# Kernel tuning notes

Hardware: AMD Instinct MI355X
Metric: run time of the kernel (lower is better)

## Reference

```python
import jax, jax.numpy as jnp
import numpy as np

H = 4096        # hidden_size
NH = 32         # num_attention_heads
NKV = 8         # num_key_value_heads
HD = H // NH    # head_dim = 128
N_REP = NH // NKV
SCALE = HD ** -0.5


def _rope(x, cos, sin):
    # x: (B, h, S, HD); cos/sin: (S, HD//2) broadcast over batch/heads
    x1 = x[..., 0::2]
    x2 = x[..., 1::2]
    return jnp.concatenate([x1 * cos - x2 * sin, x1 * sin + x2 * cos], axis=-1)


def setup_inputs() -> dict:
    key = jax.random.key(0)
    ks = jax.random.split(key, 9)
    B, S = 2, 2048
    return {
        "hidden_states": jax.random.normal(ks[0], (B, S, H), jnp.float32),
        "cos": jax.random.uniform(ks[1], (S, HD // 2), jnp.float32),
        "sin": jax.random.uniform(ks[2], (S, HD // 2), jnp.float32),
        "Wq": jax.random.normal(ks[3], (H, H), jnp.float32) * (H ** -0.5),
        "Wk": jax.random.normal(ks[4], (NKV * HD, H), jnp.float32) * (H ** -0.5),
        "bk": jax.random.normal(ks[5], (NKV * HD,), jnp.float32) * 0.01,
        "Wv": jax.random.normal(ks[6], (NKV * HD, H), jnp.float32) * (H ** -0.5),
        "bv": jax.random.normal(ks[7], (NKV * HD,), jnp.float32) * 0.01,
        "Wo": jax.random.normal(ks[8], (H, H), jnp.float32) * (H ** -0.5),
    }


def reference(hidden_states, cos, sin, Wq, Wk, bk, Wv, bv, Wo):
    B, S, _ = hidden_states.shape
    # projections (torch Linear: x @ W.T + b)
    q = (hidden_states @ Wq.T).reshape(B, S, NH, HD).transpose(0, 2, 1, 3)
    k = (hidden_states @ Wk.T + bk).reshape(B, S, NKV, HD).transpose(0, 2, 1, 3)
    v = (hidden_states @ Wv.T + bv).reshape(B, S, NKV, HD).transpose(0, 2, 1, 3)
    q = _rope(q, cos, sin)
    k = _rope(k, cos, sin)
    # GQA repeat_kv: (B, NKV, S, HD) -> (B, NH, S, HD)
    k = jnp.repeat(k, N_REP, axis=1)
    v = jnp.repeat(v, N_REP, axis=1)
    # full attention (no mask is actually applied in the source forward)
    scores = jnp.einsum('bhqd,bhkd->bhqk', q, k) * SCALE
    attn = jax.nn.softmax(scores, axis=-1)
    out = jnp.einsum('bhqk,bhkd->bhqd', attn, v)
    out = out.transpose(0, 2, 1, 3).reshape(B, S, H)
    return out @ Wo.T
```

## Files before the change

### kernel.cpp

```cpp
#include <hip/hip_runtime.h>

typedef unsigned short u16;
typedef short short8 __attribute__((ext_vector_type(8)));
typedef float floatx4 __attribute__((ext_vector_type(4)));

#define H_ 4096
#define NH_ 32
#define NKV_ 8
#define HD_ 128
#define SEQ_ 2048
#define BATCH_ 2
#define ROWS_ (BATCH_*SEQ_)
#define KVW_ (NKV_*HD_)
#define NQKV_ (H_ + 2*KVW_)
#define VSTRIDE_ NQKV_
#define SCALE_ 0.08838834764831845f
#define TSCALE_ (SCALE_*1.442695040888963f)

__device__ __forceinline__ u16 f2bf(float f) {
  union { float f; unsigned u; } x; x.f = f;
  unsigned r = x.u + 0x7fffu + ((x.u >> 16) & 1u);
  return (u16)(r >> 16);
}
__device__ __forceinline__ float bf2f(u16 h) {
  union { unsigned u; float f; } x; x.u = ((unsigned)h) << 16;
  return x.f;
}
__device__ __forceinline__ unsigned cvt_pk_bf16(float lo, float hi) {
  unsigned r;
  asm("v_cvt_pk_bf16_f32 %0, %1, %2" : "=v"(r) : "v"(lo), "v"(hi));
  return r;
}

__global__ __launch_bounds__(256) void cvt_f32_bf16(const float* __restrict__ src,
                                                    u16* __restrict__ dst, int n4) {
  int i = blockIdx.x * 256 + threadIdx.x;
  if (i >= n4) return;
  float4 v = ((const float4*)src)[i];
  ushort4 o;
  o.x = f2bf(v.x); o.y = f2bf(v.y); o.z = f2bf(v.z); o.w = f2bf(v.w);
  ((ushort4*)dst)[i] = o;
}

__global__ __launch_bounds__(256) void bias_concat(const float* __restrict__ bk,
                                                   const float* __restrict__ bv,
                                                   float* __restrict__ dst) {
  int i = blockIdx.x * 256 + threadIdx.x;
  if (i >= NQKV_) return;
  float v = 0.f;
  if (i >= H_ + KVW_)      v = bv[i - (H_ + KVW_)];
  else if (i >= H_)        v = bk[i - H_];
  dst[i] = v;
}

template<int BF16_OUT, int HAS_BIAS>
__global__ __launch_bounds__(512, 2) void gemm_nt_8p(const u16* __restrict__ A, const u16* __restrict__ B,
                                                     const float* __restrict__ bias, void* __restrict__ Cout,
                                                     int M, int N, int K)
{
  __shared__ __align__(16) u16 lds[65536];
  char* ldsB = (char*)lds;
  const int tid  = threadIdx.x;
  const int lane = tid & 63;
  const int wave = tid >> 6;
  const int ln   = lane & 15;
  const int quad = lane >> 4;
  const int wm   = wave >> 2;
  const int wn   = wave & 3;

  const int NB  = N >> 8;
  const int nwg = gridDim.x;
  const int cpx = nwg >> 3;
  const int l   = (blockIdx.x & 7) * cpx + (blockIdx.x >> 3);
  const int m0  = (l / NB) * 256;
  const int n0  = (l % NB) * 256;

  const u16* srcp[4][2];
  {
    int ob0 = wave*2048 + lane*16;
#pragma unroll
    for (int h = 0; h < 4; ++h) {
#pragma unroll
      for (int j = 0; j < 2; ++j) {
        int ob  = ob0 + j*1024;
        int row = ob >> 6;
        int sl  = ((ob >> 4) & 3) ^ ((row >> 1) & 3);
        int kst = h >> 1;
        if ((h & 1) == 0) srcp[h][j] = A + (size_t)(m0 + row)*K + kst*32 + sl*8;
        else              srcp[h][j] = B + (size_t)(n0 + row)*K + kst*32 + sl*8;
      }
    }
  }

#define STAGE(h_, p_, kt_)                                                          \
  {                                                                                 \
    __builtin_amdgcn_global_load_lds(                                               \
      (const __attribute__((address_space(1))) void*)(srcp[h_][0] + (kt_)*64),      \
      (__attribute__((address_space(3))) void*)(ldsB + (((h_)&1)*65536 + (p_)*32768 \
          + ((h_)>>1)*16384 + wave*2048)), 16, 0, 0);                               \
    __builtin_amdgcn_global_load_lds(                                               \
      (const __attribute__((address_space(1))) void*)(srcp[h_][1] + (kt_)*64),      \
      (__attribute__((address_space(3))) void*)(ldsB + (((h_)&1)*65536 + (p_)*32768 \
          + ((h_)>>1)*16384 + wave*2048 + 1024)), 16, 0, 0);                        \
  }

  const int slq16 = (quad ^ ((ln >> 1) & 3)) * 16;
  const int aoffL = (wm*128 + ln)*64 + slq16;
  const int boffL = (wn*64  + ln)*64 + slq16;

  floatx4 zf = {0.f, 0.f, 0.f, 0.f};
  floatx4 acc[8][4];
#pragma unroll
  for (int i = 0; i < 8; ++i)
#pragma unroll
    for (int j = 0; j < 4; ++j) acc[i][j] = zf;

  STAGE(0, 0, 0) STAGE(1, 0, 0) STAGE(2, 0, 0) STAGE(3, 0, 0)

  const int NT = K >> 6;
  for (int t = 0; t < NT; ++t) {
    const int p  = t & 1;
    const int np = p ^ 1;
    const char* ab = ldsB + p*32768;
    const char* bb = ldsB + 65536 + p*32768;
    short8 af[4], bq[4];

    asm volatile("s_waitcnt vmcnt(4)");
    __builtin_amdgcn_s_barrier();
    __builtin_amdgcn_sched_barrier(0);
    if (t + 1 < NT) STAGE(0, np, t+1)
#pragma unroll
    for (int j = 0; j < 4; ++j) bq[j] = *(const short8*)(bb + boffL + j*1024);
#pragma unroll
    for (int i = 0; i < 4; ++i) af[i] = *(const short8*)(ab + aoffL + i*1024);
    __builtin_amdgcn_s_setprio(1);
#pragma unroll
    for (int i = 0; i < 4; ++i)
#pragma unroll
      for (int j = 0; j < 4; ++j)
        acc[i][j] = __builtin_amdgcn_mfma_f32_16x16x32_bf16(af[i], bq[j], acc[i][j], 0, 0, 0);
    __builtin_amdgcn_s_setprio(0);

    __builtin_amdgcn_s_barrier();
    if (t + 1 < NT) STAGE(1, np, t+1)
#pragma unroll
    for (int i = 0; i < 4; ++i) af[i] = *(const short8*)(ab + aoffL + (4+i)*1024);
    __builtin_amdgcn_s_setprio(1);
#pragma unroll
    for (int i = 0; i < 4; ++i)
#pragma unroll
      for (int j = 0; j < 4; ++j)
        acc[4+i][j] = __builtin_amdgcn_mfma_f32_16x16x32_bf16(af[i], bq[j], acc[4+i][j], 0, 0, 0);
    __builtin_amdgcn_s_setprio(0);

    if (t + 1 < NT) { asm volatile("s_waitcnt vmcnt(4)"); }
    else            { asm volatile("s_waitcnt vmcnt(0)"); }
    __builtin_amdgcn_s_barrier();
    __builtin_amdgcn_sched_barrier(0);
    if (t + 1 < NT) STAGE(2, np, t+1)
#pragma unroll
    for (int j = 0; j < 4; ++j) bq[j] = *(const short8*)(bb + 16384 + boffL + j*1024);
#pragma unroll
    for (int i = 0; i < 4; ++i) af[i] = *(const short8*)(ab + 16384 + aoffL + i*1024);
    __builtin_amdgcn_s_setprio(1);
#pragma unroll
    for (int i = 0; i < 4; ++i)
#pragma unroll
      for (int j = 0; j < 4; ++j)
        acc[i][j] = __builtin_amdgcn_mfma_f32_16x16x32_bf16(af[i], bq[j], acc[i][j], 0, 0, 0);
    __builtin_amdgcn_s_setprio(0);

    __builtin_amdgcn_s_barrier();
    if (t + 1 < NT) STAGE(3, np, t+1)
#pragma unroll
    for (int i = 0; i < 4; ++i) af[i] = *(const short8*)(ab + 16384 + aoffL + (4+i)*1024);
    __builtin_amdgcn_s_setprio(1);
#pragma unroll
    for (int i = 0; i < 4; ++i)
#pragma unroll
      for (int j = 0; j < 4; ++j)
        acc[4+i][j] = __builtin_amdgcn_mfma_f32_16x16x32_bf16(af[i], bq[j], acc[4+i][j], 0, 0, 0);
    __builtin_amdgcn_s_setprio(0);
  }
#undef STAGE

#pragma unroll
  for (int i = 0; i < 8; ++i) {
#pragma unroll
    for (int j = 0; j < 4; ++j) {
      int row = m0 + wm*128 + i*16 + quad*4;
      int col = n0 + wn*64  + j*16 + ln;
      float bv_ = HAS_BIAS ? bias[col] : 0.f;
#pragma unroll
      for (int r = 0; r < 4; ++r) {
        float v = acc[i][j][r] + bv_;
        if (BF16_OUT) ((u16*)Cout)[(size_t)(row+r)*N + col] = f2bf(v);
        else          ((float*)Cout)[(size_t)(row+r)*N + col] = v;
      }
    }
  }
}

__global__ __launch_bounds__(256) void rope_kernel(const u16* __restrict__ X, u16* __restrict__ Y,
                                                   const float* __restrict__ cosb, const float* __restrict__ sinb,
                                                   int nheads, int total, int istride, int ostride)
{
  int idx = blockIdx.x * 256 + threadIdx.x;
  if (idx >= total) return;
  int d = idx & 63;
  int t = idx >> 6;
  int hh = t % nheads;
  int row = t / nheads;
  int s = row & (SEQ_ - 1);
  size_t bi = (size_t)row * istride + hh * HD_;
  size_t bo = (size_t)row * ostride + hh * HD_;
  float x1 = bf2f(X[bi + 2*d]);
  float x2 = bf2f(X[bi + 2*d + 1]);
  float c  = cosb[s*64 + d];
  float sn = sinb[s*64 + d];
  Y[bo + d]      = f2bf(x1*c - x2*sn);
  Y[bo + 64 + d] = f2bf(x1*sn + x2*c);
}

#define KS_TILE (64*128)

__global__ __launch_bounds__(256, 3) void attn_fwd(const u16* __restrict__ Q, const u16* __restrict__ K,
                                                   const u16* __restrict__ V, u16* __restrict__ O)
{
  __shared__ __align__(16) u16 Ks[2*KS_TILE];
  __shared__ __align__(16) u16 Vt[128*72];
  const int tid  = threadIdx.x;
  const int lane = tid & 63;
  const int wave = tid >> 6;
  const int ln   = lane & 15;
  const int quad = lane >> 4;
  const int bh = blockIdx.y;
  const int b  = bh >> 5;
  const int h  = bh & 31;
  const int kvh = h >> 2;
  const int q0 = blockIdx.x * 128;

  short8 qf[2][4];
#pragma unroll
  for (int mt = 0; mt < 2; ++mt) {
    const u16* qbase = Q + (size_t)(b*SEQ_ + q0 + wave*32 + mt*16 + ln) * H_ + h * HD_;
#pragma unroll
    for (int kst = 0; kst < 4; ++kst)
      qf[mt][kst] = *(const short8*)(qbase + kst*32 + quad*8);
  }

  short8 bones;
  {
    short v1 = (ln == 0) ? (short)0x3F80 : (short)0;
#pragma unroll
    for (int j = 0; j < 8; ++j) bones[j] = v1;
  }

  int kou[4];
  const u16* ks0[4];
#pragma unroll
  for (int i = 0; i < 4; ++i) {
    int ou = wave*4096 + i*1024;
    int ob = ou + lane*16;
    int key = ob >> 8;
    int dgp = (ob >> 4) & 15;
    int dgl = dgp ^ (key & 15);
    kou[i] = ou;
    ks0[i] = K + (size_t)(b*SEQ_ + key)*KVW_ + kvh*HD_ + dgl*8;
  }
  const int g  = tid & 15;
  const int dg = tid >> 4;
  const u16* vs0 = V + (size_t)(b*SEQ_ + g)*VSTRIDE_ + kvh*HD_ + dg*8;
  const int k0v = ((g >> 1) & 1)*32 + (g >> 2)*8 + (g & 1)*4;

  floatx4 zf = {0.f, 0.f, 0.f, 0.f};
  floatx4 o[2][8];
  floatx4 ol[2];
#pragma unroll
  for (int mt = 0; mt < 2; ++mt) {
    ol[mt] = zf;
#pragma unroll
    for (int jt = 0; jt < 8; ++jt) o[mt][jt] = zf;
  }
  float mrow[2] = {-1e30f, -1e30f};

  int4 vreg[4];
#pragma unroll
  for (int i = 0; i < 4; ++i)
    __builtin_amdgcn_global_load_lds((const __attribute__((address_space(1))) void*)ks0[i],
        (__attribute__((address_space(3))) void*)((char*)Ks + kou[i]), 16, 0, 0);
#pragma unroll
  for (int j = 0; j < 4; ++j)
    vreg[j] = *(const int4*)(vs0 + (size_t)(j*16)*VSTRIDE_);
  {
    union { int4 v; u16 u[8]; } w[4];
#pragma unroll
    for (int j = 0; j < 4; ++j) w[j].v = vreg[j];
#pragma unroll
    for (int dd = 0; dd < 8; ++dd) {
      ushort4 t4;
      t4.x = w[0].u[dd]; t4.y = w[1].u[dd]; t4.z = w[2].u[dd]; t4.w = w[3].u[dd];
      *(ushort4*)&Vt[(dg*8 + dd)*72 + k0v] = t4;
    }
  }
  __syncthreads();

  const int NT = SEQ_ / 64;
  for (int t = 0; t < NT; ++t) {
    if (t + 1 < NT) {
      size_t roff = (size_t)(t+1) * 64 * KVW_;
      char* kb = (char*)Ks + ((t+1)&1) * (KS_TILE*2);
#pragma unroll
      for (int i = 0; i < 4; ++i)
        __builtin_amdgcn_global_load_lds((const __attribute__((address_space(1))) void*)(ks0[i] + roff),
            (__attribute__((address_space(3))) void*)(kb + kou[i]), 16, 0, 0);
      size_t voff = (size_t)(t+1) * 64 * VSTRIDE_;
#pragma unroll
      for (int j = 0; j < 4; ++j)
        vreg[j] = *(const int4*)(vs0 + voff + (size_t)(j*16)*VSTRIDE_);
    }
    const u16* Kc = Ks + (t&1)*KS_TILE;

    floatx4 s[2][4];
#pragma unroll
    for (int nt = 0; nt < 4; ++nt) { s[0][nt] = zf; s[1][nt] = zf; }
    __builtin_amdgcn_s_setprio(1);
#pragma unroll
    for (int kst = 0; kst < 4; ++kst) {
      int dgp = (kst*4 + quad) ^ ln;
#pragma unroll
      for (int nt = 0; nt < 4; ++nt) {
        short8 kf = *(const short8*)&Kc[(nt*16 + ln)*128 + dgp*8];
        s[0][nt] = __builtin_amdgcn_mfma_f32_16x16x32_bf16(kf, qf[0][kst], s[0][nt], 0, 0, 0);
        s[1][nt] = __builtin_amdgcn_mfma_f32_16x16x32_bf16(kf, qf[1][kst], s[1][nt], 0, 0, 0);
      }
    }
    __builtin_amdgcn_s_setprio(0);

    float rmv[2];
    bool ok = true;
#pragma unroll
    for (int mt = 0; mt < 2; ++mt) {
      float m0_ = fmaxf(fmaxf(s[mt][0][0], s[mt][0][1]), fmaxf(s[mt][0][2], s[mt][0][3]));
      float m1_ = fmaxf(fmaxf(s[mt][1][0], s[mt][1][1]), fmaxf(s[mt][1][2], s[mt][1][3]));
      float m2_ = fmaxf(fmaxf(s[mt][2][0], s[mt][2][1]), fmaxf(s[mt][2][2], s[mt][2][3]));
      float m3_ = fmaxf(fmaxf(s[mt][3][0], s[mt][3][1]), fmaxf(s[mt][3][2], s[mt][3][3]));
      float rm = fmaxf(fmaxf(m0_, m1_), fmaxf(m2_, m3_)) * TSCALE_;
      rm = fmaxf(rm, __shfl_xor(rm, 16));
      rm = fmaxf(rm, __shfl_xor(rm, 32));
      rmv[mt] = rm;
      ok = ok && (rm - mrow[mt] <= 8.0f);
    }
    if (!__all(ok)) {
#pragma unroll
      for (int mt = 0; mt < 2; ++mt) {
        float mn = fmaxf(mrow[mt], rmv[mt]);
        float al = exp2f(mrow[mt] - mn);
        mrow[mt] = mn;
        float av[4];
#pragma unroll
        for (int r = 0; r < 4; ++r) av[r] = __shfl(al, (lane & 48) | (quad*4 + r));
#pragma unroll
        for (int r = 0; r < 4; ++r) {
          float a_ = av[r];
#pragma unroll
          for (int jt = 0; jt < 8; ++jt) o[mt][jt][r] *= a_;
          ol[mt][r] *= a_;
        }
      }
    }
    short8 pa[2][2];
#pragma unroll
    for (int mt = 0; mt < 2; ++mt) {
      float mn = mrow[mt];
      float p[4][4];
#pragma unroll
      for (int nt = 0; nt < 4; ++nt)
#pragma unroll
        for (int r = 0; r < 4; ++r)
          p[r][nt] = exp2f(fmaf(s[mt][nt][r], TSCALE_, -mn));
#pragma unroll
      for (int k2 = 0; k2 < 2; ++k2) {
        union { unsigned u[4]; short8 v; } pk;
        pk.u[0] = cvt_pk_bf16(p[2*k2][0],   p[2*k2][1]);
        pk.u[1] = cvt_pk_bf16(p[2*k2][2],   p[2*k2][3]);
        pk.u[2] = cvt_pk_bf16(p[2*k2+1][0], p[2*k2+1][1]);
        pk.u[3] = cvt_pk_bf16(p[2*k2+1][2], p[2*k2+1][3]);
        pa[mt][k2] = pk.v;
      }
    }

    __builtin_amdgcn_s_setprio(1);
#pragma unroll
    for (int k2 = 0; k2 < 2; ++k2) {
#pragma unroll
      for (int jt = 0; jt < 8; ++jt) {
        short8 vf = *(const short8*)&Vt[(jt*16 + ln)*72 + k2*32 + quad*8];
        o[0][jt] = __builtin_amdgcn_mfma_f32_16x16x32_bf16(pa[0][k2], vf, o[0][jt], 0, 0, 0);
        o[1][jt] = __builtin_amdgcn_mfma_f32_16x16x32_bf16(pa[1][k2], vf, o[1][jt], 0, 0, 0);
      }
      ol[0] = __builtin_amdgcn_mfma_f32_16x16x32_bf16(pa[0][k2], bones, ol[0], 0, 0, 0);
      ol[1] = __builtin_amdgcn_mfma_f32_16x16x32_bf16(pa[1][k2], bones, ol[1], 0, 0, 0);
    }
    __builtin_amdgcn_s_setprio(0);

    __syncthreads();
    if (t + 1 < NT) {
      union { int4 v; u16 u[8]; } w[4];
#pragma unroll
      for (int j = 0; j < 4; ++j) w[j].v = vreg[j];
#pragma unroll
      for (int dd = 0; dd < 8; ++dd) {
        ushort4 t4;
        t4.x = w[0].u[dd]; t4.y = w[1].u[dd]; t4.z = w[2].u[dd]; t4.w = w[3].u[dd];
        *(ushort4*)&Vt[(dg*8 + dd)*72 + k0v] = t4;
      }
    }
    __syncthreads();
  }

#pragma unroll
  for (int mt = 0; mt < 2; ++mt) {
#pragma unroll
    for (int r = 0; r < 4; ++r) {
      float lv = __shfl(ol[mt][r], lane & 48);
      float inv = 1.f / lv;
      size_t row = (size_t)(b*SEQ_ + q0 + wave*32 + mt*16 + quad*4 + r);
      u16* dst = O + row * H_ + h * HD_ + ln;
#pragma unroll
      for (int jt = 0; jt < 8; ++jt)
        dst[jt*16] = f2bf(o[mt][jt][r] * inv);
    }
  }
}

extern "C" void kernel_launch(void* const* d_in, const int* in_sizes, int n_in,
                              void* d_out, int out_size, void* d_ws, size_t ws_size,
                              hipStream_t stream) {
  const float* hs   = (const float*)d_in[0];
  const float* cosb = (const float*)d_in[1];
  const float* sinb = (const float*)d_in[2];
  const float* Wq   = (const float*)d_in[3];
  const float* Wk   = (const float*)d_in[4];
  const float* bk   = (const float*)d_in[5];
  const float* Wv   = (const float*)d_in[6];
  const float* bv   = (const float*)d_in[7];
  const float* Wo   = (const float*)d_in[8];
  float* out = (float*)d_out;

  char* ws = (char*)d_ws;
  u16*   hs_bf   = (u16*)(ws +          0);
  u16*   Wqkv_bf = (u16*)(ws +   33554432);
  u16*   Wo_bf   = (u16*)(ws +   83886080);
  u16*   QKV0    = (u16*)(ws +  117440512);
  u16*   Qr      = (u16*)(ws +  167772160);
  u16*   Kr      = (u16*)(ws +  201326592);
  float* biasqkv = (float*)(ws + 209715200);
  u16*   Oa      = hs_bf;

  {
    int n;
    n = ROWS_*H_;  cvt_f32_bf16<<<(n/4 + 255)/256, 256, 0, stream>>>(hs, hs_bf, n/4);
    n = H_*H_;     cvt_f32_bf16<<<(n/4 + 255)/256, 256, 0, stream>>>(Wq, Wqkv_bf, n/4);
    n = KVW_*H_;   cvt_f32_bf16<<<(n/4 + 255)/256, 256, 0, stream>>>(Wk, Wqkv_bf + (size_t)H_*H_, n/4);
    n = KVW_*H_;   cvt_f32_bf16<<<(n/4 + 255)/256, 256, 0, stream>>>(Wv, Wqkv_bf + (size_t)(H_+KVW_)*H_, n/4);
    n = H_*H_;     cvt_f32_bf16<<<(n/4 + 255)/256, 256, 0, stream>>>(Wo, Wo_bf, n/4);
    bias_concat<<<(NQKV_ + 255)/256, 256, 0, stream>>>(bk, bv, biasqkv);
  }

  gemm_nt_8p<1,1><<<dim3((ROWS_/256)*(NQKV_/256)), dim3(512), 0, stream>>>(hs_bf, Wqkv_bf, biasqkv, QKV0, ROWS_, NQKV_, H_);
  rope_kernel<<<(ROWS_*NH_*64)/256,  256, 0, stream>>>(QKV0,       Qr, cosb, sinb, NH_,  ROWS_*NH_*64,  NQKV_, H_);
  rope_kernel<<<(ROWS_*NKV_*64)/256, 256, 0, stream>>>(QKV0 + H_,  Kr, cosb, sinb, NKV_, ROWS_*NKV_*64, NQKV_, KVW_);
  attn_fwd<<<dim3(SEQ_/128, BATCH_*NH_), dim3(256), 0, stream>>>(Qr, Kr, QKV0 + H_ + KVW_, Oa);
  gemm_nt_8p<0,0><<<dim3((ROWS_/256)*(H_/256)), dim3(512), 0, stream>>>(Oa, Wo_bf, nullptr, out, ROWS_, H_, H_);
}
```

Measured before the change: 917.3 us.

## Double attention block to 8 waves covering 256 queries with swizzled grid mapping

The attention kernel now launches 512 threads (8 waves) per block, so each block handles 256 query rows and amortizes each K/V tile load over twice as many queries, halving per-thread K and V staging work. The grid is flattened to 512 blocks, and block indices are remapped so that consecutive blocks spread across (batch, head, query-tile) in an interleaved order, presumably for better L2 locality or XCD distribution. The launch bound changes from (256,3) to (512,4), which tightens the register budget and risks spills. There are also fewer blocks for load balancing across CUs.

```diff
diff --git a/kernel.cpp b/kernel.cpp
--- a/kernel.cpp
+++ b/kernel.cpp
@@ -224,7 +224,7 @@
 
 #define KS_TILE (64*128)
 
-__global__ __launch_bounds__(256, 3) void attn_fwd(const u16* __restrict__ Q, const u16* __restrict__ K,
+__global__ __launch_bounds__(512, 4) void attn_fwd(const u16* __restrict__ Q, const u16* __restrict__ K,
                                                    const u16* __restrict__ V, u16* __restrict__ O)
 {
   __shared__ __align__(16) u16 Ks[2*KS_TILE];
@@ -234,11 +234,12 @@
   const int wave = tid >> 6;
   const int ln   = lane & 15;
   const int quad = lane >> 4;
-  const int bh = blockIdx.y;
-  const int b  = bh >> 5;
-  const int h  = bh & 31;
+  const int lin = (blockIdx.x & 7) * 64 + (blockIdx.x >> 3);
+  const int bh  = lin >> 3;
+  const int b   = bh >> 5;
+  const int h   = bh & 31;
   const int kvh = h >> 2;
-  const int q0 = blockIdx.x * 128;
+  const int q0  = (lin & 7) * 256;
 
   short8 qf[2][4];
 #pragma unroll
@@ -256,11 +257,11 @@
     for (int j = 0; j < 8; ++j) bones[j] = v1;
   }
 
-  int kou[4];
-  const u16* ks0[4];
-#pragma unroll
-  for (int i = 0; i < 4; ++i) {
-    int ou = wave*4096 + i*1024;
+  int kou[2];
+  const u16* ks0[2];
+#pragma unroll
+  for (int i = 0; i < 2; ++i) {
+    int ou = wave*2048 + i*1024;
     int ob = ou + lane*16;
     int key = ob >> 8;
     int dgp = (ob >> 4) & 15;
@@ -269,9 +270,10 @@
     ks0[i] = K + (size_t)(b*SEQ_ + key)*KVW_ + kvh*HD_ + dgl*8;
   }
   const int g  = tid & 15;
-  const int dg = tid >> 4;
-  const u16* vs0 = V + (size_t)(b*SEQ_ + g)*VSTRIDE_ + kvh*HD_ + dg*8;
-  const int k0v = ((g >> 1) & 1)*32 + (g >> 2)*8 + (g & 1)*4;
+  const int dg = (tid >> 4) & 15;
+  const int j2 = tid >> 8;
+  const u16* vs0 = V + (size_t)(b*SEQ_ + j2*32 + g)*VSTRIDE_ + kvh*HD_ + dg*8;
+  const int k0v = ((g >> 1) & 1)*32 + (g >> 2)*8 + (g & 1)*4 + j2*2;
 
   floatx4 zf = {0.f, 0.f, 0.f, 0.f};
   floatx4 o[2][8];
@@ -284,23 +286,21 @@
   }
   float mrow[2] = {-1e30f, -1e30f};
 
-  int4 vreg[4];
-#pragma unroll
-  for (int i = 0; i < 4; ++i)
+  int4 vreg[2];
+#pragma unroll
+  for (int i = 0; i < 2; ++i)
     __builtin_amdgcn_global_load_lds((const __attribute__((address_space(1))) void*)ks0[i],
         (__attribute__((address_space(3))) void*)((char*)Ks + kou[i]), 16, 0, 0);
 #pragma unroll
-  for (int j = 0; j < 4; ++j)
-    vreg[j] = *(const int4*)(vs0 + (size_t)(j*16)*VSTRIDE_);
+  for (int jj = 0; jj < 2; ++jj)
+    vreg[jj] = *(const int4*)(vs0 + (size_t)(jj*16)*VSTRIDE_);
   {
-    union { int4 v; u16 u[8]; } w[4];
-#pragma unroll
-    for (int j = 0; j < 4; ++j) w[j].v = vreg[j];
+    union { int4 v; u16 u[8]; } w[2];
+    w[0].v = vreg[0]; w[1].v = vreg[1];
 #pragma unroll
     for (int dd = 0; dd < 8; ++dd) {
-      ushort4 t4;
-      t4.x = w[0].u[dd]; t4.y = w[1].u[dd]; t4.z = w[2].u[dd]; t4.w = w[3].u[dd];
-      *(ushort4*)&Vt[(dg*8 + dd)*72 + k0v] = t4;
+      ushort2 t2; t2.x = w[0].u[dd]; t2.y = w[1].u[dd];
+      *(ushort2*)&Vt[(dg*8 + dd)*72 + k0v] = t2;
     }
   }
   __syncthreads();
@@ -311,13 +311,13 @@
       size_t roff = (size_t)(t+1) * 64 * KVW_;
       char* kb = (char*)Ks + ((t+1)&1) * (KS_TILE*2);
 #pragma unroll
-      for (int i = 0; i < 4; ++i)
+      for (int i = 0; i < 2; ++i)
         __builtin_amdgcn_global_load_lds((const __attribute__((address_space(1))) void*)(ks0[i] + roff),
             (__attribute__((address_space(3))) void*)(kb + kou[i]), 16, 0, 0);
       size_t voff = (size_t)(t+1) * 64 * VSTRIDE_;
 #pragma unroll
-      for (int j = 0; j < 4; ++j)
-        vreg[j] = *(const int4*)(vs0 + voff + (size_t)(j*16)*VSTRIDE_);
+      for (int jj = 0; jj < 2; ++jj)
+        vreg[jj] = *(const int4*)(vs0 + voff + (size_t)(jj*16)*VSTRIDE_);
     }
     const u16* Kc = Ks + (t&1)*KS_TILE;
 
@@ -406,14 +406,12 @@
 
     __syncthreads();
     if (t + 1 < NT) {
-      union { int4 v; u16 u[8]; } w[4];
-#pragma unroll
-      for (int j = 0; j < 4; ++j) w[j].v = vreg[j];
+      union { int4 v; u16 u[8]; } w[2];
+      w[0].v = vreg[0]; w[1].v = vreg[1];
 #pragma unroll
       for (int dd = 0; dd < 8; ++dd) {
-        ushort4 t4;
-        t4.x = w[0].u[dd]; t4.y = w[1].u[dd]; t4.z = w[2].u[dd]; t4.w = w[3].u[dd];
-        *(ushort4*)&Vt[(dg*8 + dd)*72 + k0v] = t4;
+        ushort2 t2; t2.x = w[0].u[dd]; t2.y = w[1].u[dd];
+        *(ushort2*)&Vt[(dg*8 + dd)*72 + k0v] = t2;
       }
     }
     __syncthreads();
@@ -471,6 +469,6 @@
   gemm_nt_8p<1,1><<<dim3((ROWS_/256)*(NQKV_/256)), dim3(512), 0, stream>>>(hs_bf, Wqkv_bf, biasqkv, QKV0, ROWS_, NQKV_, H_);
   rope_kernel<<<(ROWS_*NH_*64)/256,  256, 0, stream>>>(QKV0,       Qr, cosb, sinb, NH_,  ROWS_*NH_*64,  NQKV_, H_);
   rope_kernel<<<(ROWS_*NKV_*64)/256, 256, 0, stream>>>(QKV0 + H_,  Kr, cosb, sinb, NKV_, ROWS_*NKV_*64, NQKV_, KVW_);
-  attn_fwd<<<dim3(SEQ_/128, BATCH_*NH_), dim3(256), 0, stream>>>(Qr, Kr, QKV0 + H_ + KVW_, Oa);
+  attn_fwd<<<dim3(512), dim3(512), 0, stream>>>(Qr, Kr, QKV0 + H_ + KVW_, Oa);
   gemm_nt_8p<0,0><<<dim3((ROWS_/256)*(H_/256)), dim3(512), 0, stream>>>(Oa, Wo_bf, nullptr, out, ROWS_, H_, H_);
 }
```

Result: slower. 948.0 us (+3.3%).
